# Performance work log

Measured on AMD Instinct MI355X. Metric: run time of the kernel, lower is better.

The kernel has to match this reference:

```python
import jax, jax.numpy as jnp
import numpy as np

B, N, M, D, H, K, V = 2, 2048, 2048, 1024, 16, 64, 64
MAX_WAVELENGTH = 10000
SCALE_FACTOR = 1.0


def rope(x, positions, max_wavelength, scale_factor):
    # x: [b, s, h, k]; positions: [b, s] int
    head_dim = x.shape[-1]
    fraction = 2.0 * jnp.arange(head_dim // 2, dtype=x.dtype) / head_dim
    timescale = jnp.asarray(max_wavelength, x.dtype) ** fraction            # [k/2]
    # scaled positions -> phase per (b, s, 1 head bcast, k/2)
    phase = (positions.astype(x.dtype) / scale_factor)[:, :, None, None] / timescale  # [b,s,1,k/2]
    sin, cos = jnp.sin(phase), jnp.cos(phase)
    x1, x2 = jnp.split(x, 2, axis=-1)
    return jnp.concatenate([x1 * cos - x2 * sin, x2 * cos + x1 * sin], axis=-1)


def setup_inputs() -> dict:
    key = jax.random.key(0)
    ks = jax.random.split(key, 8)
    scale = 1.0 / np.sqrt(D)  # keep logits numerically sane with random params
    inp = {
        "query": jax.random.normal(ks[0], (B, N, D), jnp.float32),
        "q_positions": jnp.broadcast_to(jnp.arange(N, dtype=jnp.int32), (B, N)),
        "key": jax.random.normal(ks[1], (B, M, D), jnp.float32),
        "k_positions": jnp.broadcast_to(jnp.arange(M, dtype=jnp.int32), (B, M)),
        "value": jax.random.normal(ks[2], (B, M, D), jnp.float32),
        "mask": jnp.ones((1, 1, N, M), dtype=bool),
        "P_q": jax.random.normal(ks[3], (H, D, K), jnp.float32) * scale,
        "P_k": jax.random.normal(ks[4], (H, D, K), jnp.float32) * scale,
        "P_v": jax.random.normal(ks[5], (H, D, V), jnp.float32) * scale,
        "P_o": jax.random.normal(ks[6], (H, D, V), jnp.float32) * scale,
    }
    return inp


def reference(query, q_positions, key, k_positions, value, mask, P_q, P_k, P_v, P_o):
    q = jnp.einsum('bnd,hdk->bnhk', query, P_q)
    k = jnp.einsum('bmd,hdk->bmhk', key, P_k)
    v = jnp.einsum('bmd,hdv->bmhv', value, P_v)
    q = rope(q, q_positions, MAX_WAVELENGTH, SCALE_FACTOR)
    k = rope(k, k_positions, MAX_WAVELENGTH, SCALE_FACTOR)
    logits = jnp.einsum('bnhk,bmhk->bhnm', q, k)
    if mask is not None:
        logits = jnp.where(mask, logits, -jnp.inf)
    weights = jax.nn.softmax(logits, axis=-1)
    o = jnp.einsum('bhnm,bmhv->bnhv', weights, v)
    return jnp.einsum('bnhv,hdv->bnd', o, P_o)
```

## Files before the change

### kernel.cpp

```cpp
#include <hip/hip_runtime.h>
#include <hip/hip_bf16.h>
#include <math.h>

#define B_ 2
#define N_ 2048
#define M_ 2048
#define D_ 1024
#define H_ 16


typedef _Float16 f16;
typedef f16  f16x2 __attribute__((ext_vector_type(2)));
typedef f16  f16x4 __attribute__((ext_vector_type(4)));
typedef f16  f16x8 __attribute__((ext_vector_type(8)));
typedef float f32x4  __attribute__((ext_vector_type(4)));
typedef float f32x16 __attribute__((ext_vector_type(16)));

#define MFMA16(a, b, c) __builtin_amdgcn_mfma_f32_16x16x32_f16((a), (b), (c), 0, 0, 0)
#define MFMA32(a, b, c) __builtin_amdgcn_mfma_f32_32x32x16_f16((a), (b), (c), 0, 0, 0)
#define LDST 72
#define EXP2(x) __builtin_amdgcn_exp2f(x)

#define GLOAD_LDS(g, l)                                             \
  __builtin_amdgcn_global_load_lds(                                 \
      (const __attribute__((address_space(1))) void*)(g),           \
      (__attribute__((address_space(3))) void*)(l), 16, 0, 0)

static __device__ __forceinline__ unsigned int pk2(float a, float b) {
  auto h = __builtin_amdgcn_cvt_pkrtz(a, b);
  return __builtin_bit_cast(unsigned int, h);
}
static __device__ __forceinline__ float max3f(float a, float b, float c) {
  return fmaxf(fmaxf(a, b), c);
}

__global__ __launch_bounds__(256) void prep_all(
    const float* __restrict__ Pq, const float* __restrict__ Pk,
    const float* __restrict__ Pv, const float* __restrict__ Po,
    const int* __restrict__ qpos, const int* __restrict__ kpos,
    const float* __restrict__ Aq, const float* __restrict__ Ak,
    const float* __restrict__ Av,
    f16* __restrict__ Ptq, f16* __restrict__ Ptk, f16* __restrict__ Ptv,
    f16* __restrict__ Wo, float2* __restrict__ tabq, float2* __restrict__ tabk,
    f16* __restrict__ A16q, f16* __restrict__ A16k, f16* __restrict__ A16v)
{
  __shared__ float Ts[64][65];
  const int z = blockIdx.y, x = blockIdx.x, tid = threadIdx.x;
  if (z < 3) {
    if (x >= 256) return;
    const float* P = (z == 0) ? Pq : (z == 1) ? Pk : Pv;
    f16* Pt = (z == 0) ? Ptq : (z == 1) ? Ptk : Ptv;
    const int d0 = (x & 15) * 64, h = x >> 4;
    #pragma unroll
    for (int it = 0; it < 4; ++it) {
      int fi = tid + 256 * it;
      int dr = fi >> 4, c4 = (fi & 15) << 2;
      float4 v = *(const float4*)(P + ((size_t)h * D_ + d0 + dr) * 64 + c4);
      Ts[dr][c4+0] = v.x; Ts[dr][c4+1] = v.y; Ts[dr][c4+2] = v.z; Ts[dr][c4+3] = v.w;
    }
    __syncthreads();
    const int c = tid >> 2, dp = (tid & 3) * 16;
    f16x8 w0, w1;
    #pragma unroll
    for (int i = 0; i < 8; ++i) { w0[i] = (f16)Ts[dp + i][c]; w1[i] = (f16)Ts[dp + 8 + i][c]; }
    f16* dst = Pt + ((size_t)h * 64 + c) * D_ + d0 + dp;
    *(f16x8*)dst = w0;
    *(f16x8*)(dst + 8) = w1;
  } else if (z == 3) {
    int e = (x * 256 + tid) * 4;
    if (e >= H_ * D_ * 64) return;
    int h = e >> 16, d = (e >> 6) & 1023, v = e & 63;
    float4 xx = *(const float4*)(Po + e);
    f16x4 w = {(f16)xx.x, (f16)xx.y, (f16)xx.z, (f16)xx.w};
    *(f16x4*)&Wo[(size_t)d * 1024 + h * 64 + v] = w;
  } else if (z < 6) {
    if (x >= 512) return;
    int idx = x * 256 + tid;
    int r = idx >> 5, c = idx & 31;
    const int* pos = (z == 4) ? qpos : kpos;
    float2* tab = (z == 4) ? tabq : tabk;
    float fpos = (float)pos[r];
    float inv_ts = exp2f(-(float)c * 0.4152410118609203f);
    float ph = fpos * inv_ts, sn, cs;
    sincosf(ph, &sn, &cs);
    tab[idx] = make_float2(cs, sn);
  } else {
    const float* s = (z == 6) ? Aq : (z == 7) ? Ak : Av;
    f16* d = (z == 6) ? A16q : (z == 7) ? A16k : A16v;
    size_t e = ((size_t)x * 256 + tid) * 16;
    #pragma unroll
    for (int half = 0; half < 2; ++half) {
      float4 v0 = *(const float4*)(s + e + half * 8);
      float4 v1 = *(const float4*)(s + e + half * 8 + 4);
      f16x8 w = {(f16)v0.x, (f16)v0.y, (f16)v0.z, (f16)v0.w,
                 (f16)v1.x, (f16)v1.y, (f16)v1.z, (f16)v1.w};
      *(f16x8*)(d + e + half * 8) = w;
    }
  }
}

__global__ __launch_bounds__(256) void gemm_fused(
    const f16* __restrict__ Aq, const f16* __restrict__ Ak,
    const f16* __restrict__ Av,
    const f16* __restrict__ Bq, const f16* __restrict__ Bk,
    const f16* __restrict__ Bv,
    const float2* __restrict__ tabq, const float2* __restrict__ tabk,
    f16* __restrict__ dq, f16* __restrict__ dk, f16* __restrict__ dv)
{
  __shared__ f16 As[2][128 * 64];
  __shared__ f16 Bs[2][128 * 64];
  const int tid = threadIdx.x, lane = tid & 63, wave = tid >> 6;
  const int quad = lane >> 4, l16 = lane & 15;
  const int lb = blockIdx.x + 8 * (int)blockIdx.y;
  const int xcd = lb & 7, t = lb >> 3;
  const int col0 = (t & 7) * 128;
  const int row0 = (xcd * 4 + (t >> 3)) * 128;
  const int op = blockIdx.z;
  const int wr = (wave >> 1) * 64, wc = (wave & 1) * 64;

  const f16* A  = (op == 0) ? Aq : (op == 1) ? Ak : Av;
  const f16* Bt = (op == 0) ? Bq : (op == 1) ? Bk : Bv;

  f32x4 acc[4][4] = {};
  const int srow = wave * 8 + (lane >> 3);
  const int scol = ((lane & 7) ^ ((lane >> 3) & 7)) * 8;
  const int sdst = wave * 512 + lane * 8;
  const int rx   = l16 & 7;

#define STAGE_F(b, kk)                                                       \
  _Pragma("unroll")                                                          \
  for (int c = 0; c < 4; ++c) {                                              \
    GLOAD_LDS(A  + (size_t)(row0 + c * 32 + srow) * 1024 + (kk) + scol,      \
              &As[b][c * 2048 + sdst]);                                      \
    GLOAD_LDS(Bt + (size_t)(col0 + c * 32 + srow) * 1024 + (kk) + scol,      \
              &Bs[b][c * 2048 + sdst]);                                      \
  }

#define COMPUTE_F(b)                                                         \
  _Pragma("unroll")                                                          \
  for (int ks = 0; ks < 2; ++ks) {                                           \
    f16x8 af[4], bf[4];                                                      \
    _Pragma("unroll")                                                        \
    for (int i = 0; i < 4; ++i)                                              \
      af[i] = *(const f16x8*)&As[b][(wr + i * 16 + l16) * 64 +               \
                                    ((ks * 4 + quad) ^ rx) * 8];             \
    _Pragma("unroll")                                                        \
    for (int j = 0; j < 4; ++j)                                              \
      bf[j] = *(const f16x8*)&Bs[b][(wc + j * 16 + l16) * 64 +               \
                                    ((ks * 4 + quad) ^ rx) * 8];             \
    __builtin_amdgcn_s_setprio(1);                                           \
    _Pragma("unroll")                                                        \
    for (int i = 0; i < 4; ++i)                                              \
      _Pragma("unroll")                                                      \
      for (int j = 0; j < 4; ++j)                                            \
        acc[i][j] = MFMA16(af[i], bf[j], acc[i][j]);                         \
    __builtin_amdgcn_s_setprio(0);                                           \
  }

  STAGE_F(0, 0);
  __syncthreads();
  for (int k0 = 0; k0 < 1024; k0 += 128) {
    STAGE_F(1, k0 + 64);
    COMPUTE_F(0);
    __syncthreads();
    if (k0 + 128 < 1024) STAGE_F(0, k0 + 128);
    COMPUTE_F(1);
    __syncthreads();
  }
#undef STAGE_F
#undef COMPUTE_F

  if (op == 2) {
    #pragma unroll
    for (int i = 0; i < 4; ++i) {
      int r = row0 + wr + i * 16 + quad * 4;
      int b = r >> 11, s = r & 2047;
      #pragma unroll
      for (int j = 0; j < 4; ++j) {
        int col = col0 + wc + j * 16 + l16;
        int h = col >> 6, v = col & 63;
        f16x4 w = {(f16)acc[i][j][0], (f16)acc[i][j][1],
                   (f16)acc[i][j][2], (f16)acc[i][j][3]};
        *(f16x4*)&dv[((size_t)(b * H_ + h) * 64 + v) * 2048 + s] = w;
      }
    }
  } else {
    const float2* tab = (op == 0) ? tabq : tabk;
    f16* oq = (op == 0) ? dq : dk;
    #pragma unroll
    for (int i = 0; i < 4; ++i) {
      #pragma unroll
      for (int reg = 0; reg < 4; ++reg) {
        int r = row0 + wr + i * 16 + quad * 4 + reg;
        int b = r >> 11, s = r & 2047;
        #pragma unroll
        for (int j = 0; j < 2; ++j) {
          int col = col0 + wc + j * 16 + l16;
          int h = col >> 6, c = col & 63;
          float2 cs = tab[r * 32 + c];
          float x1 = acc[i][j][reg], x2 = acc[i][j + 2][reg];
          size_t base = ((size_t)(b * H_ + h) * 2048 + s) * 64;
          oq[base + c]      = (f16)(x1 * cs.x - x2 * cs.y);
          oq[base + c + 32] = (f16)(x2 * cs.x + x1 * cs.y);
        }
      }
    }
  }
}

__global__ __launch_bounds__(512, 4) void flash7b(
    const f16* __restrict__ q, const f16* __restrict__ k,
    const f16* __restrict__ vt, f16* __restrict__ o)
{
  __shared__ __align__(16) char smem[4 * 64 * LDST * sizeof(f16)];

  const int tid = threadIdx.x, lane = tid & 63, wave = tid >> 6;
  const int g = wave >> 2, w4 = wave & 3;
  const int L = lane >> 5, nl = lane & 31;
  const int lin = blockIdx.x + 16 * (blockIdx.y + 16 * (int)blockIdx.z);
  const int xcd = lin & 7, t = lin >> 3;
  const int hb = xcd * 4 + (t >> 4);
  const int n0 = (t & 15) * 128;
  const int h = hb & 15, b = hb >> 4;

  f16* Ks  = (f16*)smem + (size_t)g * (64 * LDST);
  f16* Vts = (f16*)smem + (size_t)(2 + g) * (64 * LDST);

  const f16* qb = q  + (size_t)(b * H_ + h) * N_ * 64;
  const f16* kb = k  + (size_t)(b * H_ + h) * M_ * 64 + (size_t)g * 1024 * 64;
  const f16* vb = vt + (size_t)(b * H_ + h) * 64 * M_ + g * 1024;

  f16x8 qf[4];
  #pragma unroll
  for (int gg = 0; gg < 4; ++gg)
    qf[gg] = *(const f16x8*)(qb + (size_t)(n0 + w4 * 32 + nl) * 64 + gg * 16 + L * 8);

  f32x16 acc[2] = {};
  float mst = -INFINITY;
  float lst = 0.f;
  const float L2E = 1.4426950408889634f;

  const int gtid = tid & 255;
  const int srow = gtid >> 2, soff = (gtid & 3) * 16;

  f16x8 kp0 = *(const f16x8*)(kb + (size_t)srow * 64 + soff);
  f16x8 kp1 = *(const f16x8*)(kb + (size_t)srow * 64 + soff + 8);
  f16x8 vp0 = *(const f16x8*)(vb + (size_t)srow * M_ + soff);
  f16x8 vp1 = *(const f16x8*)(vb + (size_t)srow * M_ + soff + 8);

  for (int m0 = 0; m0 < 1024; m0 += 64) {
    __syncthreads();
    *(f16x8*)&Ks[srow * LDST + soff]      = kp0;
    *(f16x8*)&Ks[srow * LDST + soff + 8]  = kp1;
    *(f16x8*)&Vts[srow * LDST + soff]     = vp0;
    *(f16x8*)&Vts[srow * LDST + soff + 8] = vp1;
    __syncthreads();
    if (m0 + 64 < 1024) {
      kp0 = *(const f16x8*)(kb + (size_t)(m0 + 64 + srow) * 64 + soff);
      kp1 = *(const f16x8*)(kb + (size_t)(m0 + 64 + srow) * 64 + soff + 8);
      vp0 = *(const f16x8*)(vb + (size_t)srow * M_ + m0 + 64 + soff);
      vp1 = *(const f16x8*)(vb + (size_t)srow * M_ + m0 + 64 + soff + 8);
    }

    f32x16 s[2] = {};
    __builtin_amdgcn_s_setprio(1);
    #pragma unroll
    for (int u = 0; u < 2; ++u)
      #pragma unroll
      for (int gg = 0; gg < 4; ++gg) {
        f16x8 af = *(const f16x8*)&Ks[(u * 32 + nl) * LDST + gg * 16 + L * 8];
        s[u] = MFMA32(af, qf[gg], s[u]);
      }
    __builtin_amdgcn_s_setprio(0);

    float a11[11];
    #pragma unroll
    for (int i = 0; i < 10; ++i) {
      int j = 3 * i;
      float x0 = (j < 16) ? s[0][j] : s[1][j - 16];
      float x1 = (j + 1 < 16) ? s[0][j + 1] : s[1][j - 15];
      float x2 = (j + 2 < 16) ? s[0][j + 2] : s[1][j - 14];
      a11[i] = max3f(x0, x1, x2);
    }
    a11[10] = fmaxf(s[1][14], s[1][15]);
    float b4_0 = max3f(a11[0], a11[1], a11[2]);
    float b4_1 = max3f(a11[3], a11[4], a11[5]);
    float b4_2 = max3f(a11[6], a11[7], a11[8]);
    float b4_3 = fmaxf(a11[9], a11[10]);
    float mx = fmaxf(fmaxf(b4_0, b4_1), fmaxf(b4_2, b4_3));
    mx = fmaxf(mx, __shfl_xor(mx, 32));
    float mx2 = mx * L2E;
    float m_new = fmaxf(mst, mx2);

    if (!__all(mx2 - mst <= 8.0f)) {
      float alpha = EXP2(mst - m_new);
      #pragma unroll
      for (int u = 0; u < 2; ++u)
        #pragma unroll
        for (int r = 0; r < 16; ++r) acc[u][r] *= alpha;
      lst *= alpha;
      mst = m_new;
    }

    #pragma unroll
    for (int u = 0; u < 2; ++u)
      #pragma unroll
      for (int r = 0; r < 16; ++r)
        s[u][r] = EXP2(s[u][r] * L2E - mst);

    unsigned int qw[2][4][2];
    #pragma unroll
    for (int u = 0; u < 2; ++u)
      #pragma unroll
      for (int rq = 0; rq < 4; ++rq) {
        qw[u][rq][0] = pk2(s[u][rq * 4 + 0], s[u][rq * 4 + 1]);
        qw[u][rq][1] = pk2(s[u][rq * 4 + 2], s[u][rq * 4 + 3]);
      }

#if __has_builtin(__builtin_amdgcn_fdot2)
    {
      const f16x2 one2 = {(f16)1.0f, (f16)1.0f};
      float sum = 0.f;
      #pragma unroll
      for (int u = 0; u < 2; ++u)
        #pragma unroll
        for (int rq = 0; rq < 4; ++rq)
          #pragma unroll
          for (int w = 0; w < 2; ++w)
            sum = __builtin_amdgcn_fdot2(
                __builtin_bit_cast(f16x2, qw[u][rq][w]), one2, sum, false);
      sum += __shfl_xor(sum, 32);
      lst += sum;
    }
#else
    {
      float ts[16];
      #pragma unroll
      for (int r = 0; r < 16; ++r) ts[r] = s[0][r] + s[1][r];
      #pragma unroll
      for (int st = 8; st >= 1; st >>= 1)
        #pragma unroll
        for (int r = 0; r < st; ++r) ts[r] += ts[r + st];
      float sum = ts[0];
      sum += __shfl_xor(sum, 32);
      lst += sum;
    }
#endif

    union PBu { unsigned int w[4]; f16x8 v; } pb[4];
    #pragma unroll
    for (int u = 0; u < 2; ++u)
      #pragma unroll
      for (int gg = 0; gg < 2; ++gg)
        #pragma unroll
        for (int w = 0; w < 2; ++w) {
          unsigned int a = qw[u][2 * gg][w], bb = qw[u][2 * gg + 1][w];
          asm volatile("v_permlane32_swap_b32 %0, %1" : "+v"(a), "+v"(bb));
          pb[2 * u + gg].w[w]     = a;
          pb[2 * u + gg].w[2 + w] = bb;
        }

    __builtin_amdgcn_s_setprio(1);
    #pragma unroll
    for (int u = 0; u < 2; ++u)
      #pragma unroll
      for (int gg = 0; gg < 4; ++gg) {
        f16x8 vf = *(const f16x8*)&Vts[(u * 32 + nl) * LDST + gg * 16 + L * 8];
        acc[u] = MFMA32(vf, pb[gg].v, acc[u]);
      }
    __builtin_amdgcn_s_setprio(0);
  }

  float* mrg = (float*)smem;
  const int mb = (w4 * 64 + lane) * 34;
  __syncthreads();
  if (g == 1) {
    #pragma unroll
    for (int r = 0; r < 16; ++r) { mrg[mb + r] = acc[0][r]; mrg[mb + 16 + r] = acc[1][r]; }
    mrg[mb + 32] = mst;
    mrg[mb + 33] = lst;
  }
  __syncthreads();
  if (g == 0) {
    float m1 = mrg[mb + 32], l1 = mrg[mb + 33];
    float Mm = fmaxf(mst, m1);
    float a0 = EXP2(mst - Mm), a1 = EXP2(m1 - Mm);
    float invl = 1.0f / (a0 * lst + a1 * l1);
    f16* ob = o + ((size_t)(b * N_ + n0 + w4 * 32 + nl) * 1024) + h * 64;
    #pragma unroll
    for (int u = 0; u < 2; ++u)
      #pragma unroll
      for (int rq = 0; rq < 4; ++rq) {
        f16x4 w;
        #pragma unroll
        for (int j = 0; j < 4; ++j)
          w[j] = (f16)((a0 * acc[u][rq * 4 + j] + a1 * mrg[mb + u * 16 + rq * 4 + j]) * invl);
        *(f16x4*)&ob[u * 32 + 8 * rq + 4 * L] = w;
      }
  }
}

__global__ __launch_bounds__(256) void gemm_out(
    const f16* __restrict__ A, const f16* __restrict__ Bt,
    float* __restrict__ out)
{
  __shared__ f16 As[2][128 * 64];
  __shared__ f16 Bs[2][64 * 64];
  const int tid = threadIdx.x, lane = tid & 63, wave = tid >> 6;
  const int quad = lane >> 4, l16 = lane & 15;
  const int lb = blockIdx.x + 16 * (int)blockIdx.y;
  const int xcd = lb & 7, t = lb >> 3;
  const int col0 = (t & 15) * 64;
  const int row0 = (xcd * 4 + (t >> 4)) * 128;
  const int wr = (wave >> 1) * 64, wc = (wave & 1) * 32;

  f32x4 acc[4][2] = {};
  const int srow = wave * 8 + (lane >> 3);
  const int scol = ((lane & 7) ^ ((lane >> 3) & 7)) * 8;
  const int sdst = wave * 512 + lane * 8;
  const int rx   = l16 & 7;

#define STAGE_O(b, kk)                                                       \
  _Pragma("unroll")                                                          \
  for (int c = 0; c < 4; ++c)                                                \
    GLOAD_LDS(A + (size_t)(row0 + c * 32 + srow) * 1024 + (kk) + scol,       \
              &As[b][c * 2048 + sdst]);                                      \
  _Pragma("unroll")                                                          \
  for (int c = 0; c < 2; ++c)                                                \
    GLOAD_LDS(Bt + (size_t)(col0 + c * 32 + srow) * 1024 + (kk) + scol,      \
              &Bs[b][c * 2048 + sdst]);

#define COMPUTE_O(b)                                                         \
  _Pragma("unroll")                                                          \
  for (int ks = 0; ks < 2; ++ks) {                                           \
    f16x8 af[4], bf[2];                                                      \
    _Pragma("unroll")                                                        \
    for (int i = 0; i < 4; ++i)                                              \
      af[i] = *(const f16x8*)&As[b][(wr + i * 16 + l16) * 64 +               \
                                    ((ks * 4 + quad) ^ rx) * 8];             \
    _Pragma("unroll")                                                        \
    for (int j = 0; j < 2; ++j)                                              \
      bf[j] = *(const f16x8*)&Bs[b][(wc + j * 16 + l16) * 64 +               \
                                    ((ks * 4 + quad) ^ rx) * 8];             \
    __builtin_amdgcn_s_setprio(1);                                           \
    _Pragma("unroll")                                                        \
    for (int i = 0; i < 4; ++i)                                              \
      _Pragma("unroll")                                                      \
      for (int j = 0; j < 2; ++j)                                            \
        acc[i][j] = MFMA16(af[i], bf[j], acc[i][j]);                         \
    __builtin_amdgcn_s_setprio(0);                                           \
  }

  STAGE_O(0, 0);
  __syncthreads();
  for (int k0 = 0; k0 < 1024; k0 += 128) {
    STAGE_O(1, k0 + 64);
    COMPUTE_O(0);
    __syncthreads();
    if (k0 + 128 < 1024) STAGE_O(0, k0 + 128);
    COMPUTE_O(1);
    __syncthreads();
  }
#undef STAGE_O
#undef COMPUTE_O

  #pragma unroll
  for (int i = 0; i < 4; ++i)
    #pragma unroll
    for (int j = 0; j < 2; ++j)
      #pragma unroll
      for (int reg = 0; reg < 4; ++reg)
        out[(size_t)(row0 + wr + i * 16 + quad * 4 + reg) * 1024 +
            col0 + wc + j * 16 + l16] = acc[i][j][reg];
}

extern "C" void kernel_launch(void* const* d_in, const int* in_sizes, int n_in,
                              void* d_out, int out_size, void* d_ws, size_t ws_size,
                              hipStream_t stream) {
  (void)in_sizes; (void)n_in; (void)out_size; (void)ws_size;
  const float* query = (const float*)d_in[0];
  const int*   qpos  = (const int*)d_in[1];
  const float* key   = (const float*)d_in[2];
  const int*   kpos  = (const int*)d_in[3];
  const float* value = (const float*)d_in[4];
  const float* Pq = (const float*)d_in[6];
  const float* Pk = (const float*)d_in[7];
  const float* Pv = (const float*)d_in[8];
  const float* Po = (const float*)d_in[9];
  float* out = (float*)d_out;

  const size_t pm = (size_t)1024 * 1024;
  const size_t em = (size_t)B_ * H_ * 2048 * 64;
  f16* Ptq = (f16*)d_ws;
  f16* Ptk = Ptq + pm;
  f16* Ptv = Ptk + pm;
  f16* Wo  = Ptv + pm;
  f16* q_ws  = Wo + pm;
  f16* k_ws  = q_ws + em;
  f16* vt_ws = k_ws + em;
  f16* o_ws  = vt_ws + em;
  float2* tabq = (float2*)(o_ws + em);
  float2* tabk = tabq + (size_t)4096 * 32;
  f16* a16q = (f16*)(tabk + (size_t)4096 * 32);
  f16* a16k = a16q + em;
  f16* a16v = a16k + em;

  dim3 blk(256);
  prep_all<<<dim3(1024, 9), blk, 0, stream>>>(
      Pq, Pk, Pv, Po, qpos, kpos, query, key, value,
      Ptq, Ptk, Ptv, Wo, tabq, tabk, a16q, a16k, a16v);

  gemm_fused<<<dim3(8, 32, 3), blk, 0, stream>>>(
      a16q, a16k, a16v, Ptq, Ptk, Ptv, tabq, tabk, q_ws, k_ws, vt_ws);

  flash7b<<<dim3(N_ / 128, H_, B_), dim3(512), 0, stream>>>(q_ws, k_ws, vt_ws, o_ws);

  gemm_out<<<dim3(16, 32), blk, 0, stream>>>(o_ws, Wo, out);
}
```

Before: 225.5 us.

## Fold log2e into Q projection and compute softmax row sums with MFMA

The log2(e) factor is now applied to Q in the projection epilogue, which removes a per-element multiply from the softmax exponent and max computation in the attention loop. The row-sum of the probabilities, previously built with fdot2 accumulations and a cross-lane shuffle, is now produced by an extra MFMA against a vector of ones into a separate accumulator. The scalar work moves onto the matrix unit at the cost of 16 more accumulator registers and four extra MFMAs per tile, which may increase register pressure at this occupancy. Scaling Q before the fp16 cast also changes its rounding slightly.

```diff
diff --git a/kernel.cpp b/kernel.cpp
--- a/kernel.cpp
+++ b/kernel.cpp
@@ -187,6 +187,7 @@
   } else {
     const float2* tab = (op == 0) ? tabq : tabk;
     f16* oq = (op == 0) ? dq : dk;
+    const float qs = (op == 0) ? 1.4426950408889634f : 1.0f;
     #pragma unroll
     for (int i = 0; i < 4; ++i) {
       #pragma unroll
@@ -200,15 +201,15 @@
           float2 cs = tab[r * 32 + c];
           float x1 = acc[i][j][reg], x2 = acc[i][j + 2][reg];
           size_t base = ((size_t)(b * H_ + h) * 2048 + s) * 64;
-          oq[base + c]      = (f16)(x1 * cs.x - x2 * cs.y);
-          oq[base + c + 32] = (f16)(x2 * cs.x + x1 * cs.y);
+          oq[base + c]      = (f16)((x1 * cs.x - x2 * cs.y) * qs);
+          oq[base + c + 32] = (f16)((x2 * cs.x + x1 * cs.y) * qs);
         }
       }
     }
   }
 }
 
-__global__ __launch_bounds__(512, 4) void flash7b(
+__global__ __launch_bounds__(512, 4) void flash7d(
     const f16* __restrict__ q, const f16* __restrict__ k,
     const f16* __restrict__ vt, f16* __restrict__ o)
 {
@@ -236,9 +237,10 @@
     qf[gg] = *(const f16x8*)(qb + (size_t)(n0 + w4 * 32 + nl) * 64 + gg * 16 + L * 8);
 
   f32x16 acc[2] = {};
+  f32x16 sacc = {};
   float mst = -INFINITY;
-  float lst = 0.f;
-  const float L2E = 1.4426950408889634f;
+  const f16 one_h = (f16)1.0f;
+  const f16x8 ones8 = {one_h, one_h, one_h, one_h, one_h, one_h, one_h, one_h};
 
   const int gtid = tid & 255;
   const int srow = gtid >> 2, soff = (gtid & 3) * 16;
@@ -289,16 +291,16 @@
     float b4_3 = fmaxf(a11[9], a11[10]);
     float mx = fmaxf(fmaxf(b4_0, b4_1), fmaxf(b4_2, b4_3));
     mx = fmaxf(mx, __shfl_xor(mx, 32));
-    float mx2 = mx * L2E;
-    float m_new = fmaxf(mst, mx2);
-
-    if (!__all(mx2 - mst <= 8.0f)) {
+    float m_new = fmaxf(mst, mx);
+
+    if (!__all(mx - mst <= 8.0f)) {
       float alpha = EXP2(mst - m_new);
       #pragma unroll
       for (int u = 0; u < 2; ++u)
         #pragma unroll
         for (int r = 0; r < 16; ++r) acc[u][r] *= alpha;
-      lst *= alpha;
+      #pragma unroll
+      for (int r = 0; r < 16; ++r) sacc[r] *= alpha;
       mst = m_new;
     }
 
@@ -306,7 +308,7 @@
     for (int u = 0; u < 2; ++u)
       #pragma unroll
       for (int r = 0; r < 16; ++r)
-        s[u][r] = EXP2(s[u][r] * L2E - mst);
+        s[u][r] = EXP2(s[u][r] - mst);
 
     unsigned int qw[2][4][2];
     #pragma unroll
@@ -316,36 +318,6 @@
         qw[u][rq][0] = pk2(s[u][rq * 4 + 0], s[u][rq * 4 + 1]);
         qw[u][rq][1] = pk2(s[u][rq * 4 + 2], s[u][rq * 4 + 3]);
       }
-
-#if __has_builtin(__builtin_amdgcn_fdot2)
-    {
-      const f16x2 one2 = {(f16)1.0f, (f16)1.0f};
-      float sum = 0.f;
-      #pragma unroll
-      for (int u = 0; u < 2; ++u)
-        #pragma unroll
-        for (int rq = 0; rq < 4; ++rq)
-          #pragma unroll
-          for (int w = 0; w < 2; ++w)
-            sum = __builtin_amdgcn_fdot2(
-                __builtin_bit_cast(f16x2, qw[u][rq][w]), one2, sum, false);
-      sum += __shfl_xor(sum, 32);
-      lst += sum;
-    }
-#else
-    {
-      float ts[16];
-      #pragma unroll
-      for (int r = 0; r < 16; ++r) ts[r] = s[0][r] + s[1][r];
-      #pragma unroll
-      for (int st = 8; st >= 1; st >>= 1)
-        #pragma unroll
-        for (int r = 0; r < st; ++r) ts[r] += ts[r + st];
-      float sum = ts[0];
-      sum += __shfl_xor(sum, 32);
-      lst += sum;
-    }
-#endif
 
     union PBu { unsigned int w[4]; f16x8 v; } pb[4];
     #pragma unroll
@@ -368,6 +340,9 @@
         f16x8 vf = *(const f16x8*)&Vts[(u * 32 + nl) * LDST + gg * 16 + L * 8];
         acc[u] = MFMA32(vf, pb[gg].v, acc[u]);
       }
+    #pragma unroll
+    for (int gg = 0; gg < 4; ++gg)
+      sacc = MFMA32(ones8, pb[gg].v, sacc);
     __builtin_amdgcn_s_setprio(0);
   }
 
@@ -378,14 +353,14 @@
     #pragma unroll
     for (int r = 0; r < 16; ++r) { mrg[mb + r] = acc[0][r]; mrg[mb + 16 + r] = acc[1][r]; }
     mrg[mb + 32] = mst;
-    mrg[mb + 33] = lst;
+    mrg[mb + 33] = sacc[0];
   }
   __syncthreads();
   if (g == 0) {
     float m1 = mrg[mb + 32], l1 = mrg[mb + 33];
     float Mm = fmaxf(mst, m1);
     float a0 = EXP2(mst - Mm), a1 = EXP2(m1 - Mm);
-    float invl = 1.0f / (a0 * lst + a1 * l1);
+    float invl = 1.0f / (a0 * sacc[0] + a1 * l1);
     f16* ob = o + ((size_t)(b * N_ + n0 + w4 * 32 + nl) * 1024) + h * 64;
     #pragma unroll
     for (int u = 0; u < 2; ++u)
@@ -513,7 +488,7 @@
   gemm_fused<<<dim3(8, 32, 3), blk, 0, stream>>>(
       a16q, a16k, a16v, Ptq, Ptk, Ptv, tabq, tabk, q_ws, k_ws, vt_ws);
 
-  flash7b<<<dim3(N_ / 128, H_, B_), dim3(512), 0, stream>>>(q_ws, k_ws, vt_ws, o_ws);
+  flash7d<<<dim3(N_ / 128, H_, B_), dim3(512), 0, stream>>>(q_ws, k_ws, vt_ws, o_ws);
 
   gemm_out<<<dim3(16, 32), blk, 0, stream>>>(o_ws, Wo, out);
 }
```

After: 253.8 us. +12.5%, slower.
